# Kernel optimization log

Measured on AMD Instinct MI355X. Metric: run time of the kernel, lower is better.

The kernel has to match this reference:

```python
import jax, jax.numpy as jnp
import numpy as np

NUM_GRAPHS = 256
NUM_LAYERS = 4
HIDDEN = 256
N_FEATS = 9
VOCAB = 119
BN_EPS = 1e-5


def setup_inputs() -> dict:
    key = jax.random.key(0)
    ks = jax.random.split(key, 16)
    N, E, H = 10000, 320000, HIDDEN
    x = jax.random.randint(ks[0], (N, N_FEATS), 0, 2, dtype=jnp.int64)
    edge_index = jax.random.randint(ks[1], (2, E), 0, N, dtype=jnp.int64)
    batch_ids = jnp.sort(jax.random.randint(ks[2], (N,), 0, NUM_GRAPHS, dtype=jnp.int64))
    s = 1.0 / np.sqrt(H)
    emb = jax.random.normal(ks[3], (N_FEATS, VOCAB, H), jnp.float32) * 0.02
    W = jax.random.normal(ks[4], (NUM_LAYERS, H, H), jnp.float32) * s
    b = jnp.zeros((NUM_LAYERS, H), jnp.float32)
    gamma = jnp.ones((NUM_LAYERS, H), jnp.float32)
    beta = jnp.zeros((NUM_LAYERS, H), jnp.float32)
    mlp_W1 = jax.random.normal(ks[5], (H, H // 2), jnp.float32) * s
    mlp_b1 = jnp.zeros((H // 2,), jnp.float32)
    mlp_W2 = jax.random.normal(ks[6], (H // 2, H // 4), jnp.float32) * (1.0 / np.sqrt(H // 2))
    mlp_b2 = jnp.zeros((H // 4,), jnp.float32)
    mlp_W3 = jax.random.normal(ks[7], (H // 4, 1), jnp.float32) * (1.0 / np.sqrt(H // 4))
    mlp_b3 = jnp.zeros((1,), jnp.float32)
    return dict(x=x, edge_index=edge_index, batch_ids=batch_ids, emb=emb, W=W, b=b,
                gamma=gamma, beta=beta, mlp_W1=mlp_W1, mlp_b1=mlp_b1,
                mlp_W2=mlp_W2, mlp_b2=mlp_b2, mlp_W3=mlp_W3, mlp_b3=mlp_b3)


def reference(x, edge_index, batch_ids, emb, W, b, gamma, beta,
              mlp_W1, mlp_b1, mlp_W2, mlp_b2, mlp_W3, mlp_b3):
    N = x.shape[0]
    src, dst = edge_index[0], edge_index[1]

    # AtomEncoder: sum of per-feature embeddings. emb[f, x[:,f]] -> [N, 9, H]
    h = jnp.sum(emb[jnp.arange(N_FEATS), x], axis=1)

    # GCN normalization with self-loops: deg_i = 1 + in-degree, norm = deg^-1/2
    deg = 1.0 + jax.ops.segment_sum(jnp.ones_like(dst, jnp.float32), dst, num_segments=N)
    nrm = jax.lax.rsqrt(deg)
    edge_w = (nrm[src] * nrm[dst])[:, None]   # [E,1]
    self_w = (nrm * nrm)[:, None]             # [N,1]

    for l in range(NUM_LAYERS):
        identity = h
        hw = h @ W[l]                                     # dense GEMM [N,H]x[H,H]
        agg = jax.ops.segment_sum(hw[src] * edge_w, dst, num_segments=N) + hw * self_w
        h = agg + b[l]
        # BatchNorm1d (training statistics over nodes)
        mu = jnp.mean(h, axis=0)
        var = jnp.var(h, axis=0)
        h = (h - mu) * jax.lax.rsqrt(var + BN_EPS) * gamma[l] + beta[l]
        h = jax.nn.relu(h)
        h = h + identity  # residual

    # global mean pool over graph ids
    sums = jax.ops.segment_sum(h, batch_ids, num_segments=NUM_GRAPHS)
    cnt = jax.ops.segment_sum(jnp.ones((N,), jnp.float32), batch_ids, num_segments=NUM_GRAPHS)
    g = sums / jnp.maximum(cnt, 1.0)[:, None]             # [G, H]

    # MLP head [H, H/2, H/4, 1]
    g = jax.nn.relu(g @ mlp_W1 + mlp_b1)
    g = jax.nn.relu(g @ mlp_W2 + mlp_b2)
    return g @ mlp_W3 + mlp_b3
```

## Files before the change

kernel.cpp:

```cpp
#include <hip/hip_runtime.h>

#define HID 256
#define NFEAT 9
#define VOCAB 119
#define NLAYERS 4
#define NGRAPHS 256
#define BN_EPS 1e-5f
#define POISON 0xAAAAAAAAu
#define CAP 128

typedef short short8 __attribute__((ext_vector_type(8)));
typedef float floatx4 __attribute__((ext_vector_type(4)));

__device__ inline unsigned short f2bf(float f) {
    unsigned int u = __float_as_uint(f);
    unsigned int r = u + 0x7FFF + ((u >> 16) & 1);
    return (unsigned short)(r >> 16);
}
__device__ inline float bf2f(unsigned short u) {
    return __uint_as_float(((unsigned int)u) << 16);
}

__global__ __launch_bounds__(256) void setup_misc(
        const int* __restrict__ x, const float* __restrict__ emb,
        const float* __restrict__ W, const int* __restrict__ src,
        const int* __restrict__ dst,
        int* __restrict__ fillc, int* __restrict__ bucket,
        unsigned short* __restrict__ wt, unsigned short* __restrict__ hbA,
        int N, int E, int nbFill) {
    const int bx = blockIdx.x;
    const int tid = threadIdx.x;
    __shared__ float sw[32][33];
    __shared__ int xf[NFEAT];

    if (bx < nbFill) {
        int i = bx * 256 + tid;
        if (i < E) {
            int d = dst[i];
            int slot = (int)((unsigned)atomicAdd(&fillc[d], 1) - POISON);
            if (slot < CAP) bucket[(size_t)d * CAP + slot] = src[i];
        }
    } else if (bx < nbFill + 256) {
        int j = bx - nbFill;
        int l = j >> 6;
        int rem = j & 63;
        int k0 = (rem >> 3) * 32, n0 = (rem & 7) * 32;
        int c = tid & 31, r8 = tid >> 5;
        const float* Wl = W + (size_t)l * HID * HID;
        unsigned short* Wtl = wt + (size_t)l * HID * HID;
#pragma unroll
        for (int p = 0; p < 4; ++p) {
            int r = r8 + p * 8;
            sw[r][c] = Wl[(k0 + r) * HID + n0 + c];
        }
        __syncthreads();
#pragma unroll
        for (int p = 0; p < 4; ++p) {
            int r = r8 + p * 8;
            Wtl[(size_t)(n0 + r) * HID + k0 + c] = f2bf(sw[c][r]);
        }
    } else {
        int n = bx - nbFill - 256;
        if (n < N) {
            if (tid < NFEAT) xf[tid] = x[n * NFEAT + tid];
            __syncthreads();
            float s = 0.f;
#pragma unroll
            for (int f = 0; f < NFEAT; ++f) s += emb[(size_t)(f * VOCAB + xf[f]) * HID + tid];
            hbA[(size_t)n * HID + tid] = f2bf(s);
        }
    }
}

template <bool FIRST>
__global__ __launch_bounds__(256) void agg_g4_kernel(const unsigned short* __restrict__ hb,
                                                     const int* __restrict__ fillc,
                                                     const int* __restrict__ bucket,
                                                     float* __restrict__ wbuf,
                                                     unsigned short* __restrict__ aggb, int N) {
    int bx = blockIdx.x;
    int half = bx & 1;
    int tid = threadIdx.x;
    int wave = tid >> 6;
    int lane = tid & 63;
    int g = lane >> 4;
    int sl = lane & 15;
    int n = (bx >> 1) * 4 + wave;
    if (n >= N) return;
    int co = half * 128 + sl * 8;
    const unsigned short* hbc = hb + co;
    size_t bbase = (size_t)n * CAP;

    int lenr = fillc[n];
    int sE0 = bucket[bbase + lane];
    float w0 = 0.f;
    if (!FIRST) w0 = wbuf[bbase + lane];
    short8 us = *(const short8*)&hbc[(size_t)n * HID];

    int len = (int)((unsigned)lenr - POISON);
    int lenc = min(len, CAP);
    float nd = 0.f, sw2;
    if (FIRST) { nd = rsqrtf(1.0f + (float)len); sw2 = nd * nd; }
    else       { sw2 = 1.0f / (1.0f + (float)len); }

    float a[8];
#pragma unroll
    for (int k = 0; k < 8; ++k) a[k] = 0.f;

    auto process = [&](int m, int sE, float wl) {
        int mq = m & ~3;
        if (mq > 0) {
            int srcn = __shfl(sE, g, 64);
            float wcur = __shfl(wl, g, 64);
            short8 ucur = *(const short8*)&hbc[(size_t)srcn * HID];
            for (int j = 4; j < mq; j += 4) {
                int jn = j + g;
                int sn = __shfl(sE, jn, 64);
                float wnx = __shfl(wl, jn, 64);
                short8 unext = *(const short8*)&hbc[(size_t)sn * HID];
#pragma unroll
                for (int k = 0; k < 8; ++k) a[k] += wcur * bf2f((unsigned short)ucur[k]);
                ucur = unext;
                wcur = wnx;
            }
#pragma unroll
            for (int k = 0; k < 8; ++k) a[k] += wcur * bf2f((unsigned short)ucur[k]);
        }
        if (mq < m) {
            int jj = mq + g;
            int cj = jj < m ? jj : (m - 1);
            int srcn = __shfl(sE, cj, 64);
            float w = __shfl(wl, cj, 64);
            if (jj >= m) w = 0.f;
            short8 u = *(const short8*)&hbc[(size_t)srcn * HID];
#pragma unroll
            for (int k = 0; k < 8; ++k) a[k] += w * bf2f((unsigned short)u[k]);
        }
    };

    int done = 0;
    if (lenc > 0) {
        int m = min(64, lenc);
        float wl;
        if (FIRST) {
            int sg = (lane < m) ? sE0 : 0;
            int dg = (int)((unsigned)fillc[sg] - POISON);
            wl = rsqrtf(1.0f + (float)dg) * nd;
            if (half == 0 && lane < m) wbuf[bbase + lane] = wl;
        } else {
            wl = w0;
        }
        process(m, sE0, wl);
        done = m;
    }
    while (done < lenc) {
        int m = min(64, lenc - done);
        int li = done + (lane < m ? lane : m - 1);
        int sE = bucket[bbase + li];
        float wl;
        if (FIRST) {
            int dg = (int)((unsigned)fillc[sE] - POISON);
            wl = rsqrtf(1.0f + (float)dg) * nd;
            if (half == 0 && lane < m) wbuf[bbase + li] = wl;
        } else {
            wl = wbuf[bbase + li];
        }
        process(m, sE, wl);
        done += m;
    }

#pragma unroll
    for (int k = 0; k < 8; ++k) {
        a[k] += __shfl_xor(a[k], 16);
        a[k] += __shfl_xor(a[k], 32);
    }
    if (g == 0) {
        short8 o;
#pragma unroll
        for (int k = 0; k < 8; ++k) {
            float v = a[k] + sw2 * bf2f((unsigned short)us[k]);
            o[k] = (short)f2bf(v);
        }
        *(short8*)&aggb[(size_t)n * HID + co] = o;
    }
}

__global__ __launch_bounds__(256) void mfma_gemm128(const unsigned short* __restrict__ A,
                                                    const unsigned short* __restrict__ Bt,
                                                    unsigned short* __restrict__ C,
                                                    float* __restrict__ sums, int M) {
    __shared__ unsigned short As[128][40];
    __shared__ unsigned short Bs[64][40];
    __shared__ float lsum[64];
    __shared__ float lsq[64];
    int tid = threadIdx.x;
    int row0 = blockIdx.x * 128;
    int col0 = blockIdx.y * 64;
    int lane = tid & 63;
    int wid = tid >> 6;
    int arow = tid >> 1;
    int akc = (tid & 1) * 16;
    int brow = tid >> 2;
    int bkc = (tid & 3) * 8;
    int wm = (wid & 1) * 64;
    int wn = (wid >> 1) * 32;
    int quad = lane >> 4;
    int ln = lane & 15;

    floatx4 acc[4][2];
#pragma unroll
    for (int r = 0; r < 4; ++r)
#pragma unroll
        for (int c = 0; c < 2; ++c) acc[r][c] = (floatx4){0.f, 0.f, 0.f, 0.f};

    if (tid < 64) { lsum[tid] = 0.f; lsq[tid] = 0.f; }

    for (int kk = 0; kk < HID; kk += 32) {
        short8 av0 = {0, 0, 0, 0, 0, 0, 0, 0};
        short8 av1 = {0, 0, 0, 0, 0, 0, 0, 0};
        int ar = row0 + arow;
        if (ar < M) {
            av0 = *(const short8*)&A[(size_t)ar * HID + kk + akc];
            av1 = *(const short8*)&A[(size_t)ar * HID + kk + akc + 8];
        }
        short8 bv = *(const short8*)&Bt[(size_t)(col0 + brow) * HID + kk + bkc];
        *(short8*)&As[arow][akc] = av0;
        *(short8*)&As[arow][akc + 8] = av1;
        *(short8*)&Bs[brow][bkc] = bv;
        __syncthreads();
        short8 bf0 = *(const short8*)&Bs[wn + ln][quad * 8];
        short8 bf1 = *(const short8*)&Bs[wn + 16 + ln][quad * 8];
#pragma unroll
        for (int r = 0; r < 4; ++r) {
            short8 af = *(const short8*)&As[wm + r * 16 + ln][quad * 8];
            acc[r][0] = __builtin_amdgcn_mfma_f32_16x16x32_bf16(af, bf0, acc[r][0], 0, 0, 0);
            acc[r][1] = __builtin_amdgcn_mfma_f32_16x16x32_bf16(af, bf1, acc[r][1], 0, 0, 0);
        }
        __syncthreads();
    }
    const int c0 = col0 + wn + ln;
    const int c1 = col0 + wn + 16 + ln;
    float p0 = 0.f, q0 = 0.f, p1 = 0.f, q1 = 0.f;
#pragma unroll
    for (int r = 0; r < 4; ++r) {
#pragma unroll
        for (int rr = 0; rr < 4; ++rr) {
            int row = row0 + wm + r * 16 + quad * 4 + rr;
            if (row < M) {
                float v0 = acc[r][0][rr];
                float v1 = acc[r][1][rr];
                C[(size_t)row * HID + c0] = f2bf(v0);
                C[(size_t)row * HID + c1] = f2bf(v1);
                p0 += v0; q0 += v0 * v0;
                p1 += v1; q1 += v1 * v1;
            }
        }
    }
    atomicAdd(&lsum[wn + ln], p0);
    atomicAdd(&lsq[wn + ln], q0);
    atomicAdd(&lsum[wn + 16 + ln], p1);
    atomicAdd(&lsq[wn + 16 + ln], q1);
    __syncthreads();
    if (tid < 64) {
        unsafeAtomicAdd(&sums[col0 + tid], lsum[tid]);
        unsafeAtomicAdd(&sums[HID + col0 + tid], lsq[tid]);
    }
}

__global__ __launch_bounds__(256) void bn_kernel(const unsigned short* __restrict__ hwb,
                                                 const float* __restrict__ sums,
                                                 const float* __restrict__ gamma,
                                                 const float* __restrict__ beta,
                                                 const unsigned short* __restrict__ hold,
                                                 unsigned short* __restrict__ hbnew, int N) {
    int i4 = blockIdx.x * blockDim.x + threadIdx.x;
    int base = i4 * 4;
    if (base >= N * HID) return;
    int c = base & (HID - 1);
    float invN = 1.0f / (float)N;
    float4 s4 = *(const float4*)&sums[c];
    float4 q4 = *(const float4*)&sums[HID + c];
    float4 g4 = *(const float4*)&gamma[c];
    float4 be4 = *(const float4*)&beta[c];
    ushort4 v = *(const ushort4*)&hwb[base];
    ushort4 r = *(const ushort4*)&hold[base];
    ushort4 o;
    {
        float mu = s4.x * invN, var = q4.x * invN - mu * mu;
        o.x = f2bf(fmaxf((bf2f(v.x) - mu) * g4.x * rsqrtf(var + BN_EPS) + be4.x, 0.f) + bf2f(r.x));
        mu = s4.y * invN; var = q4.y * invN - mu * mu;
        o.y = f2bf(fmaxf((bf2f(v.y) - mu) * g4.y * rsqrtf(var + BN_EPS) + be4.y, 0.f) + bf2f(r.y));
        mu = s4.z * invN; var = q4.z * invN - mu * mu;
        o.z = f2bf(fmaxf((bf2f(v.z) - mu) * g4.z * rsqrtf(var + BN_EPS) + be4.z, 0.f) + bf2f(r.z));
        mu = s4.w * invN; var = q4.w * invN - mu * mu;
        o.w = f2bf(fmaxf((bf2f(v.w) - mu) * g4.w * rsqrtf(var + BN_EPS) + be4.w, 0.f) + bf2f(r.w));
    }
    *(ushort4*)&hbnew[base] = o;
}

__device__ inline int lower_bound_g(const int* __restrict__ a, int n, int key) {
    int lo = 0, hi = n;
    while (lo < hi) {
        int mid = (lo + hi) >> 1;
        if (a[mid] < key) lo = mid + 1; else hi = mid;
    }
    return lo;
}

__global__ __launch_bounds__(256) void pool_mlp_bn_kernel(
        const unsigned short* __restrict__ hwb,
        const float* __restrict__ sums,
        const float* __restrict__ gamma,
        const float* __restrict__ beta,
        const unsigned short* __restrict__ resid,
        const int* __restrict__ batch, int N,
        const float* __restrict__ W1, const float* __restrict__ b1,
        const float* __restrict__ W2, const float* __restrict__ b2,
        const float* __restrict__ W3, const float* __restrict__ b3,
        float* __restrict__ out) {
    int g = blockIdx.x, tid = threadIdx.x;
    int lo = lower_bound_g(batch, N, g);
    int hi = lower_bound_g(batch, N, g + 1);
    float invN = 1.0f / (float)N;
    float mu = sums[tid] * invN;
    float var = sums[HID + tid] * invN - mu * mu;
    float sc = gamma[tid] * rsqrtf(var + BN_EPS);
    float be = beta[tid];
    float s = 0.f;
    for (int i = lo; i < hi; ++i) {
        float v = (bf2f(hwb[(size_t)i * HID + tid]) - mu) * sc + be;
        v = fmaxf(v, 0.f) + bf2f(resid[(size_t)i * HID + tid]);
        s += v;
    }
    __shared__ float gs[256];
    __shared__ float t1[128];
    __shared__ float t2[64];
    float inv = 1.0f / fmaxf((float)(hi - lo), 1.0f);
    gs[tid] = s * inv;
    __syncthreads();
    if (tid < 128) {
        float a = b1[tid];
        for (int k = 0; k < 256; ++k) a += gs[k] * W1[k * 128 + tid];
        t1[tid] = fmaxf(a, 0.f);
    }
    __syncthreads();
    if (tid < 64) {
        float a = b2[tid];
        for (int k = 0; k < 128; ++k) a += t1[k] * W2[k * 64 + tid];
        t2[tid] = fmaxf(a, 0.f);
    }
    __syncthreads();
    if (tid < 64) {
        float p = t2[tid] * W3[tid];
#pragma unroll
        for (int off = 32; off >= 1; off >>= 1) p += __shfl_down(p, off);
        if (tid == 0) out[g] = p + b3[0];
    }
}

extern "C" void kernel_launch(void* const* d_in, const int* in_sizes, int n_in,
                              void* d_out, int out_size, void* d_ws, size_t ws_size,
                              hipStream_t stream) {
    const int* x      = (const int*)d_in[0];
    const int* ei     = (const int*)d_in[1];
    const int* batch  = (const int*)d_in[2];
    const float* emb  = (const float*)d_in[3];
    const float* W    = (const float*)d_in[4];
    const float* gamma= (const float*)d_in[6];
    const float* beta = (const float*)d_in[7];
    const float* W1   = (const float*)d_in[8];
    const float* b1   = (const float*)d_in[9];
    const float* W2   = (const float*)d_in[10];
    const float* b2   = (const float*)d_in[11];
    const float* W3   = (const float*)d_in[12];
    const float* b3   = (const float*)d_in[13];
    float* out = (float*)d_out;

    int N = in_sizes[0] / NFEAT;
    int E = in_sizes[1] / 2;
    const int* srcp = ei;
    const int* dstp = ei + E;

    char* ws = (char*)d_ws;
    auto alloc = [&](size_t bytes) -> char* {
        char* p = ws;
        ws += (bytes + 255) & ~(size_t)255;
        return p;
    };
    int* fillc    = (int*)alloc((size_t)N * 4);
    int* bucket   = (int*)alloc((size_t)N * CAP * 4);
    float* wbuf   = (float*)alloc((size_t)N * CAP * 4);
    unsigned short* hbA  = (unsigned short*)alloc((size_t)N * HID * 2);
    unsigned short* hbB  = (unsigned short*)alloc((size_t)N * HID * 2);
    unsigned short* aggb = (unsigned short*)alloc((size_t)N * HID * 2);
    unsigned short* hwb  = (unsigned short*)alloc((size_t)N * HID * 2);
    unsigned short* wt   = (unsigned short*)alloc((size_t)NLAYERS * HID * HID * 2);
    float* bnsums = (float*)alloc((size_t)NLAYERS * 2 * HID * 4);

    int nbFill = (E + 255) / 256;
    int miscGrid = nbFill + 256 + N;
    setup_misc<<<miscGrid, 256, 0, stream>>>(x, emb, W, srcp, dstp, fillc, bucket, wt, hbA,
                                             N, E, nbFill);

    unsigned short* hbcur = hbA;
    unsigned short* hboth = hbB;
    int aggGrid = ((N + 3) / 4) * 2;
    dim3 ggrid((N + 127) / 128, 4);
    for (int l = 0; l < NLAYERS; ++l) {
        float* lsums = bnsums + (size_t)l * 2 * HID;
        if (l == 0)
            agg_g4_kernel<true><<<aggGrid, 256, 0, stream>>>(hbcur, fillc, bucket, wbuf, aggb, N);
        else
            agg_g4_kernel<false><<<aggGrid, 256, 0, stream>>>(hbcur, fillc, bucket, wbuf, aggb, N);
        mfma_gemm128<<<ggrid, 256, 0, stream>>>(aggb, wt + (size_t)l * HID * HID, hwb, lsums, N);
        if (l < NLAYERS - 1) {
            bn_kernel<<<((size_t)N * HID / 4 + 255) / 256, 256, 0, stream>>>(
                hwb, lsums, gamma + (size_t)l * HID, beta + (size_t)l * HID,
                hbcur, hboth, N);
            unsigned short* tb = hbcur; hbcur = hboth; hboth = tb;
        }
    }

    pool_mlp_bn_kernel<<<NGRAPHS, 256, 0, stream>>>(
        hwb, bnsums + (size_t)3 * 2 * HID, gamma + (size_t)3 * HID, beta + (size_t)3 * HID,
        hbcur, batch, N, W1, b1, W2, b2, W3, b3, out);
}
```

Before: 257.1 us.

## Reorder GEMM before aggregation and fuse BatchNorm into GEMM prologue

Each layer now runs the GEMM first and the sparse aggregation second, which is valid because aggregation is linear. BatchNorm statistics are accumulated in the aggregation kernel into 64 slotted buffers to reduce atomic contention. The standalone BN kernel is removed: the next layer's GEMM applies normalize+ReLU+residual while loading its A tile and writes the new hidden state from the y=0 column blocks. This saves one full N×H read/write pass and one launch per layer, at the cost of redundant BN arithmetic across the four column blocks and slot-reduction loads in each GEMM block. The code does not zero the slot buffers, so it relies on the workspace already being zeroed.

```diff
diff --git a/kernel.cpp b/kernel.cpp
--- a/kernel.cpp
+++ b/kernel.cpp
@@ -8,6 +8,7 @@
 #define BN_EPS 1e-5f
 #define POISON 0xAAAAAAAAu
 #define CAP 128
+#define NSLOT 64
 
 typedef short short8 __attribute__((ext_vector_type(8)));
 typedef float floatx4 __attribute__((ext_vector_type(4)));
@@ -73,11 +74,12 @@
 }
 
 template <bool FIRST>
-__global__ __launch_bounds__(256) void agg_g4_kernel(const unsigned short* __restrict__ hb,
-                                                     const int* __restrict__ fillc,
-                                                     const int* __restrict__ bucket,
-                                                     float* __restrict__ wbuf,
-                                                     unsigned short* __restrict__ aggb, int N) {
+__global__ __launch_bounds__(256) void agg_stats_kernel(
+        const unsigned short* __restrict__ hw, const int* __restrict__ fillc,
+        const int* __restrict__ bucket, float* __restrict__ wbuf,
+        unsigned short* __restrict__ z, float* __restrict__ zslot, int N) {
+    __shared__ float cs[4][128];
+    __shared__ float cq[4][128];
     int bx = blockIdx.x;
     int half = bx & 1;
     int tid = threadIdx.x;
@@ -86,113 +88,145 @@
     int g = lane >> 4;
     int sl = lane & 15;
     int n = (bx >> 1) * 4 + wave;
-    if (n >= N) return;
+    bool valid = n < N;
     int co = half * 128 + sl * 8;
-    const unsigned short* hbc = hb + co;
-    size_t bbase = (size_t)n * CAP;
-
-    int lenr = fillc[n];
-    int sE0 = bucket[bbase + lane];
-    float w0 = 0.f;
-    if (!FIRST) w0 = wbuf[bbase + lane];
-    short8 us = *(const short8*)&hbc[(size_t)n * HID];
-
-    int len = (int)((unsigned)lenr - POISON);
-    int lenc = min(len, CAP);
-    float nd = 0.f, sw2;
-    if (FIRST) { nd = rsqrtf(1.0f + (float)len); sw2 = nd * nd; }
-    else       { sw2 = 1.0f / (1.0f + (float)len); }
-
-    float a[8];
-#pragma unroll
-    for (int k = 0; k < 8; ++k) a[k] = 0.f;
-
-    auto process = [&](int m, int sE, float wl) {
-        int mq = m & ~3;
-        if (mq > 0) {
-            int srcn = __shfl(sE, g, 64);
-            float wcur = __shfl(wl, g, 64);
-            short8 ucur = *(const short8*)&hbc[(size_t)srcn * HID];
-            for (int j = 4; j < mq; j += 4) {
-                int jn = j + g;
-                int sn = __shfl(sE, jn, 64);
-                float wnx = __shfl(wl, jn, 64);
-                short8 unext = *(const short8*)&hbc[(size_t)sn * HID];
+    const unsigned short* hbc = hw + co;
+
+    float v[8];
+#pragma unroll
+    for (int k = 0; k < 8; ++k) v[k] = 0.f;
+
+    if (valid) {
+        size_t bbase = (size_t)n * CAP;
+        int lenr = fillc[n];
+        int sE0 = bucket[bbase + lane];
+        float w0 = 0.f;
+        if (!FIRST) w0 = wbuf[bbase + lane];
+        short8 us = *(const short8*)&hbc[(size_t)n * HID];
+
+        int len = (int)((unsigned)lenr - POISON);
+        int lenc = min(len, CAP);
+        float nd = 0.f, sw2;
+        if (FIRST) { nd = rsqrtf(1.0f + (float)len); sw2 = nd * nd; }
+        else       { sw2 = 1.0f / (1.0f + (float)len); }
+
+        float a[8];
+#pragma unroll
+        for (int k = 0; k < 8; ++k) a[k] = 0.f;
+
+        auto process = [&](int m, int sE, float wl) {
+            int mq = m & ~3;
+            if (mq > 0) {
+                int srcn = __shfl(sE, g, 64);
+                float wcur = __shfl(wl, g, 64);
+                short8 ucur = *(const short8*)&hbc[(size_t)srcn * HID];
+                for (int j = 4; j < mq; j += 4) {
+                    int jn = j + g;
+                    int sn = __shfl(sE, jn, 64);
+                    float wnx = __shfl(wl, jn, 64);
+                    short8 unext = *(const short8*)&hbc[(size_t)sn * HID];
+#pragma unroll
+                    for (int k = 0; k < 8; ++k) a[k] += wcur * bf2f((unsigned short)ucur[k]);
+                    ucur = unext;
+                    wcur = wnx;
+                }
 #pragma unroll
                 for (int k = 0; k < 8; ++k) a[k] += wcur * bf2f((unsigned short)ucur[k]);
-                ucur = unext;
-                wcur = wnx;
-            }
-#pragma unroll
-            for (int k = 0; k < 8; ++k) a[k] += wcur * bf2f((unsigned short)ucur[k]);
-        }
-        if (mq < m) {
-            int jj = mq + g;
-            int cj = jj < m ? jj : (m - 1);
-            int srcn = __shfl(sE, cj, 64);
-            float w = __shfl(wl, cj, 64);
-            if (jj >= m) w = 0.f;
-            short8 u = *(const short8*)&hbc[(size_t)srcn * HID];
-#pragma unroll
-            for (int k = 0; k < 8; ++k) a[k] += w * bf2f((unsigned short)u[k]);
-        }
-    };
-
-    int done = 0;
-    if (lenc > 0) {
-        int m = min(64, lenc);
-        float wl;
-        if (FIRST) {
-            int sg = (lane < m) ? sE0 : 0;
-            int dg = (int)((unsigned)fillc[sg] - POISON);
-            wl = rsqrtf(1.0f + (float)dg) * nd;
-            if (half == 0 && lane < m) wbuf[bbase + lane] = wl;
+            }
+            if (mq < m) {
+                int jj = mq + g;
+                int cj = jj < m ? jj : (m - 1);
+                int srcn = __shfl(sE, cj, 64);
+                float w = __shfl(wl, cj, 64);
+                if (jj >= m) w = 0.f;
+                short8 u = *(const short8*)&hbc[(size_t)srcn * HID];
+#pragma unroll
+                for (int k = 0; k < 8; ++k) a[k] += w * bf2f((unsigned short)u[k]);
+            }
+        };
+
+        int done = 0;
+        if (lenc > 0) {
+            int m = min(64, lenc);
+            float wl;
+            if (FIRST) {
+                int sg = (lane < m) ? sE0 : 0;
+                int dg = (int)((unsigned)fillc[sg] - POISON);
+                wl = rsqrtf(1.0f + (float)dg) * nd;
+                if (half == 0 && lane < m) wbuf[bbase + lane] = wl;
+            } else {
+                wl = w0;
+            }
+            process(m, sE0, wl);
+            done = m;
+        }
+        while (done < lenc) {
+            int m = min(64, lenc - done);
+            int li = done + (lane < m ? lane : m - 1);
+            int sE = bucket[bbase + li];
+            float wl;
+            if (FIRST) {
+                int dg = (int)((unsigned)fillc[sE] - POISON);
+                wl = rsqrtf(1.0f + (float)dg) * nd;
+                if (half == 0 && lane < m) wbuf[bbase + li] = wl;
+            } else {
+                wl = wbuf[bbase + li];
+            }
+            process(m, sE, wl);
+            done += m;
+        }
+
+#pragma unroll
+        for (int k = 0; k < 8; ++k) {
+            a[k] += __shfl_xor(a[k], 16);
+            a[k] += __shfl_xor(a[k], 32);
+        }
+#pragma unroll
+        for (int k = 0; k < 8; ++k) v[k] = a[k] + sw2 * bf2f((unsigned short)us[k]);
+    }
+
+    if (g == 0) {
+        if (valid) {
+            short8 o;
+#pragma unroll
+            for (int k = 0; k < 8; ++k) {
+                o[k] = (short)f2bf(v[k]);
+                cs[wave][sl * 8 + k] = v[k];
+                cq[wave][sl * 8 + k] = v[k] * v[k];
+            }
+            *(short8*)&z[(size_t)n * HID + co] = o;
         } else {
-            wl = w0;
-        }
-        process(m, sE0, wl);
-        done = m;
-    }
-    while (done < lenc) {
-        int m = min(64, lenc - done);
-        int li = done + (lane < m ? lane : m - 1);
-        int sE = bucket[bbase + li];
-        float wl;
-        if (FIRST) {
-            int dg = (int)((unsigned)fillc[sE] - POISON);
-            wl = rsqrtf(1.0f + (float)dg) * nd;
-            if (half == 0 && lane < m) wbuf[bbase + li] = wl;
-        } else {
-            wl = wbuf[bbase + li];
-        }
-        process(m, sE, wl);
-        done += m;
-    }
-
-#pragma unroll
-    for (int k = 0; k < 8; ++k) {
-        a[k] += __shfl_xor(a[k], 16);
-        a[k] += __shfl_xor(a[k], 32);
-    }
-    if (g == 0) {
-        short8 o;
-#pragma unroll
-        for (int k = 0; k < 8; ++k) {
-            float v = a[k] + sw2 * bf2f((unsigned short)us[k]);
-            o[k] = (short)f2bf(v);
-        }
-        *(short8*)&aggb[(size_t)n * HID + co] = o;
-    }
-}
-
-__global__ __launch_bounds__(256) void mfma_gemm128(const unsigned short* __restrict__ A,
-                                                    const unsigned short* __restrict__ Bt,
-                                                    unsigned short* __restrict__ C,
-                                                    float* __restrict__ sums, int M) {
+#pragma unroll
+            for (int k = 0; k < 8; ++k) {
+                cs[wave][sl * 8 + k] = 0.f;
+                cq[wave][sl * 8 + k] = 0.f;
+            }
+        }
+    }
+    __syncthreads();
+    if (tid < 128) {
+        float s = cs[0][tid] + cs[1][tid] + cs[2][tid] + cs[3][tid];
+        float q = cq[0][tid] + cq[1][tid] + cq[2][tid] + cq[3][tid];
+        float* zs = zslot + (size_t)(bx & (NSLOT - 1)) * 512;
+        unsafeAtomicAdd(&zs[half * 128 + tid], s);
+        unsafeAtomicAdd(&zs[256 + half * 128 + tid], q);
+    }
+}
+
+template <bool FUSE>
+__global__ __launch_bounds__(256) void mfma_gemm128(
+        const unsigned short* __restrict__ A,
+        const unsigned short* __restrict__ R,
+        const float* __restrict__ zsl,
+        const float* __restrict__ gamma, const float* __restrict__ beta,
+        const unsigned short* __restrict__ Bt,
+        unsigned short* __restrict__ C,
+        unsigned short* __restrict__ Hout,
+        int M) {
     __shared__ unsigned short As[128][40];
     __shared__ unsigned short Bs[64][40];
-    __shared__ float lsum[64];
-    __shared__ float lsq[64];
+    __shared__ float scA[256];
+    __shared__ float bA[256];
     int tid = threadIdx.x;
     int row0 = blockIdx.x * 128;
     int col0 = blockIdx.y * 64;
@@ -207,21 +241,56 @@
     int quad = lane >> 4;
     int ln = lane & 15;
 
+    if (FUSE) {
+        float s = 0.f, q = 0.f;
+#pragma unroll 8
+        for (int k2 = 0; k2 < NSLOT; ++k2) {
+            s += zsl[k2 * 512 + tid];
+            q += zsl[k2 * 512 + 256 + tid];
+        }
+        float invN = 1.0f / (float)M;
+        float mu = s * invN, var = q * invN - mu * mu;
+        float sc = gamma[tid] * rsqrtf(var + BN_EPS);
+        scA[tid] = sc;
+        bA[tid] = beta[tid] - mu * sc;
+        __syncthreads();
+    }
+
     floatx4 acc[4][2];
 #pragma unroll
     for (int r = 0; r < 4; ++r)
 #pragma unroll
         for (int c = 0; c < 2; ++c) acc[r][c] = (floatx4){0.f, 0.f, 0.f, 0.f};
-
-    if (tid < 64) { lsum[tid] = 0.f; lsq[tid] = 0.f; }
 
     for (int kk = 0; kk < HID; kk += 32) {
         short8 av0 = {0, 0, 0, 0, 0, 0, 0, 0};
         short8 av1 = {0, 0, 0, 0, 0, 0, 0, 0};
         int ar = row0 + arow;
         if (ar < M) {
-            av0 = *(const short8*)&A[(size_t)ar * HID + kk + akc];
-            av1 = *(const short8*)&A[(size_t)ar * HID + kk + akc + 8];
+            if (!FUSE) {
+                av0 = *(const short8*)&A[(size_t)ar * HID + kk + akc];
+                av1 = *(const short8*)&A[(size_t)ar * HID + kk + akc + 8];
+            } else {
+                short8 z0 = *(const short8*)&A[(size_t)ar * HID + kk + akc];
+                short8 z1 = *(const short8*)&A[(size_t)ar * HID + kk + akc + 8];
+                short8 r0 = *(const short8*)&R[(size_t)ar * HID + kk + akc];
+                short8 r1 = *(const short8*)&R[(size_t)ar * HID + kk + akc + 8];
+#pragma unroll
+                for (int j = 0; j < 8; ++j) {
+                    int c = kk + akc + j;
+                    float f = bf2f((unsigned short)z0[j]) * scA[c] + bA[c];
+                    f = fmaxf(f, 0.f) + bf2f((unsigned short)r0[j]);
+                    av0[j] = (short)f2bf(f);
+                    c += 8;
+                    f = bf2f((unsigned short)z1[j]) * scA[c] + bA[c];
+                    f = fmaxf(f, 0.f) + bf2f((unsigned short)r1[j]);
+                    av1[j] = (short)f2bf(f);
+                }
+                if (blockIdx.y == 0) {
+                    *(short8*)&Hout[(size_t)ar * HID + kk + akc] = av0;
+                    *(short8*)&Hout[(size_t)ar * HID + kk + akc + 8] = av1;
+                }
+            }
         }
         short8 bv = *(const short8*)&Bt[(size_t)(col0 + brow) * HID + kk + bkc];
         *(short8*)&As[arow][akc] = av0;
@@ -240,62 +309,17 @@
     }
     const int c0 = col0 + wn + ln;
     const int c1 = col0 + wn + 16 + ln;
-    float p0 = 0.f, q0 = 0.f, p1 = 0.f, q1 = 0.f;
 #pragma unroll
     for (int r = 0; r < 4; ++r) {
 #pragma unroll
         for (int rr = 0; rr < 4; ++rr) {
             int row = row0 + wm + r * 16 + quad * 4 + rr;
             if (row < M) {
-                float v0 = acc[r][0][rr];
-                float v1 = acc[r][1][rr];
-                C[(size_t)row * HID + c0] = f2bf(v0);
-                C[(size_t)row * HID + c1] = f2bf(v1);
-                p0 += v0; q0 += v0 * v0;
-                p1 += v1; q1 += v1 * v1;
-            }
-        }
-    }
-    atomicAdd(&lsum[wn + ln], p0);
-    atomicAdd(&lsq[wn + ln], q0);
-    atomicAdd(&lsum[wn + 16 + ln], p1);
-    atomicAdd(&lsq[wn + 16 + ln], q1);
-    __syncthreads();
-    if (tid < 64) {
-        unsafeAtomicAdd(&sums[col0 + tid], lsum[tid]);
-        unsafeAtomicAdd(&sums[HID + col0 + tid], lsq[tid]);
-    }
-}
-
-__global__ __launch_bounds__(256) void bn_kernel(const unsigned short* __restrict__ hwb,
-                                                 const float* __restrict__ sums,
-                                                 const float* __restrict__ gamma,
-                                                 const float* __restrict__ beta,
-                                                 const unsigned short* __restrict__ hold,
-                                                 unsigned short* __restrict__ hbnew, int N) {
-    int i4 = blockIdx.x * blockDim.x + threadIdx.x;
-    int base = i4 * 4;
-    if (base >= N * HID) return;
-    int c = base & (HID - 1);
-    float invN = 1.0f / (float)N;
-    float4 s4 = *(const float4*)&sums[c];
-    float4 q4 = *(const float4*)&sums[HID + c];
-    float4 g4 = *(const float4*)&gamma[c];
-    float4 be4 = *(const float4*)&beta[c];
-    ushort4 v = *(const ushort4*)&hwb[base];
-    ushort4 r = *(const ushort4*)&hold[base];
-    ushort4 o;
-    {
-        float mu = s4.x * invN, var = q4.x * invN - mu * mu;
-        o.x = f2bf(fmaxf((bf2f(v.x) - mu) * g4.x * rsqrtf(var + BN_EPS) + be4.x, 0.f) + bf2f(r.x));
-        mu = s4.y * invN; var = q4.y * invN - mu * mu;
-        o.y = f2bf(fmaxf((bf2f(v.y) - mu) * g4.y * rsqrtf(var + BN_EPS) + be4.y, 0.f) + bf2f(r.y));
-        mu = s4.z * invN; var = q4.z * invN - mu * mu;
-        o.z = f2bf(fmaxf((bf2f(v.z) - mu) * g4.z * rsqrtf(var + BN_EPS) + be4.z, 0.f) + bf2f(r.z));
-        mu = s4.w * invN; var = q4.w * invN - mu * mu;
-        o.w = f2bf(fmaxf((bf2f(v.w) - mu) * g4.w * rsqrtf(var + BN_EPS) + be4.w, 0.f) + bf2f(r.w));
-    }
-    *(ushort4*)&hbnew[base] = o;
+                C[(size_t)row * HID + c0] = f2bf(acc[r][0][rr]);
+                C[(size_t)row * HID + c1] = f2bf(acc[r][1][rr]);
+            }
+        }
+    }
 }
 
 __device__ inline int lower_bound_g(const int* __restrict__ a, int n, int key) {
@@ -308,8 +332,8 @@
 }
 
 __global__ __launch_bounds__(256) void pool_mlp_bn_kernel(
-        const unsigned short* __restrict__ hwb,
-        const float* __restrict__ sums,
+        const unsigned short* __restrict__ z,
+        const float* __restrict__ zsl,
         const float* __restrict__ gamma,
         const float* __restrict__ beta,
         const unsigned short* __restrict__ resid,
@@ -321,14 +345,20 @@
     int g = blockIdx.x, tid = threadIdx.x;
     int lo = lower_bound_g(batch, N, g);
     int hi = lower_bound_g(batch, N, g + 1);
+    float s0 = 0.f, q0 = 0.f;
+#pragma unroll 8
+    for (int k2 = 0; k2 < NSLOT; ++k2) {
+        s0 += zsl[k2 * 512 + tid];
+        q0 += zsl[k2 * 512 + 256 + tid];
+    }
     float invN = 1.0f / (float)N;
-    float mu = sums[tid] * invN;
-    float var = sums[HID + tid] * invN - mu * mu;
+    float mu = s0 * invN;
+    float var = q0 * invN - mu * mu;
     float sc = gamma[tid] * rsqrtf(var + BN_EPS);
     float be = beta[tid];
     float s = 0.f;
     for (int i = lo; i < hi; ++i) {
-        float v = (bf2f(hwb[(size_t)i * HID + tid]) - mu) * sc + be;
+        float v = (bf2f(z[(size_t)i * HID + tid]) - mu) * sc + be;
         v = fmaxf(v, 0.f) + bf2f(resid[(size_t)i * HID + tid]);
         s += v;
     }
@@ -390,38 +420,42 @@
     int* fillc    = (int*)alloc((size_t)N * 4);
     int* bucket   = (int*)alloc((size_t)N * CAP * 4);
     float* wbuf   = (float*)alloc((size_t)N * CAP * 4);
-    unsigned short* hbA  = (unsigned short*)alloc((size_t)N * HID * 2);
-    unsigned short* hbB  = (unsigned short*)alloc((size_t)N * HID * 2);
-    unsigned short* aggb = (unsigned short*)alloc((size_t)N * HID * 2);
-    unsigned short* hwb  = (unsigned short*)alloc((size_t)N * HID * 2);
-    unsigned short* wt   = (unsigned short*)alloc((size_t)NLAYERS * HID * HID * 2);
-    float* bnsums = (float*)alloc((size_t)NLAYERS * 2 * HID * 4);
+    unsigned short* hbA   = (unsigned short*)alloc((size_t)N * HID * 2);
+    unsigned short* hbB   = (unsigned short*)alloc((size_t)N * HID * 2);
+    unsigned short* zbuf  = (unsigned short*)alloc((size_t)N * HID * 2);
+    unsigned short* hwbuf = (unsigned short*)alloc((size_t)N * HID * 2);
+    unsigned short* wt    = (unsigned short*)alloc((size_t)NLAYERS * HID * HID * 2);
+    float* zslots = (float*)alloc((size_t)NLAYERS * NSLOT * 512 * 4);
 
     int nbFill = (E + 255) / 256;
     int miscGrid = nbFill + 256 + N;
     setup_misc<<<miscGrid, 256, 0, stream>>>(x, emb, W, srcp, dstp, fillc, bucket, wt, hbA,
                                              N, E, nbFill);
 
-    unsigned short* hbcur = hbA;
-    unsigned short* hboth = hbB;
+    unsigned short* hA = hbA;
+    unsigned short* hB = hbB;
     int aggGrid = ((N + 3) / 4) * 2;
     dim3 ggrid((N + 127) / 128, 4);
     for (int l = 0; l < NLAYERS; ++l) {
-        float* lsums = bnsums + (size_t)l * 2 * HID;
+        if (l == 0) {
+            mfma_gemm128<false><<<ggrid, 256, 0, stream>>>(
+                hbA, nullptr, nullptr, nullptr, nullptr,
+                wt, hwbuf, nullptr, N);
+        } else {
+            float* zslPrev = zslots + (size_t)(l - 1) * NSLOT * 512;
+            mfma_gemm128<true><<<ggrid, 256, 0, stream>>>(
+                zbuf, hA, zslPrev, gamma + (size_t)(l - 1) * HID, beta + (size_t)(l - 1) * HID,
+                wt + (size_t)l * HID * HID, hwbuf, hB, N);
+            unsigned short* t = hA; hA = hB; hB = t;
+        }
+        float* zsl = zslots + (size_t)l * NSLOT * 512;
         if (l == 0)
-            agg_g4_kernel<true><<<aggGrid, 256, 0, stream>>>(hbcur, fillc, bucket, wbuf, aggb, N);
+            agg_stats_kernel<true><<<aggGrid, 256, 0, stream>>>(hwbuf, fillc, bucket, wbuf, zbuf, zsl, N);
         else
-            agg_g4_kernel<false><<<aggGrid, 256, 0, stream>>>(hbcur, fillc, bucket, wbuf, aggb, N);
-        mfma_gemm128<<<ggrid, 256, 0, stream>>>(aggb, wt + (size_t)l * HID * HID, hwb, lsums, N);
-        if (l < NLAYERS - 1) {
-            bn_kernel<<<((size_t)N * HID / 4 + 255) / 256, 256, 0, stream>>>(
-                hwb, lsums, gamma + (size_t)l * HID, beta + (size_t)l * HID,
-                hbcur, hboth, N);
-            unsigned short* tb = hbcur; hbcur = hboth; hboth = tb;
-        }
+            agg_stats_kernel<false><<<aggGrid, 256, 0, stream>>>(hwbuf, fillc, bucket, wbuf, zbuf, zsl, N);
     }
 
     pool_mlp_bn_kernel<<<NGRAPHS, 256, 0, stream>>>(
-        hwb, bnsums + (size_t)3 * 2 * HID, gamma + (size_t)3 * HID, beta + (size_t)3 * HID,
-        hbcur, batch, N, W1, b1, W2, b2, W3, b3, out);
-}
+        zbuf, zslots + (size_t)3 * NSLOT * 512, gamma + (size_t)3 * HID, beta + (size_t)3 * HID,
+        hA , batch, N, W1, b1, W2, b2, W3, b3, out);
+}
```

Result: slower. 277.7 us (+8.0%).
